# Kernel optimization log

Hardware: AMD Instinct MI355X
Metric: run time of the kernel (lower is better)

## Reference

```python
import jax, jax.numpy as jnp
import numpy as np
import math

N_NODES = 100000
N_EDGES = 1600000
IN_DIM = 32
OUT_DIM = 32

def setup_inputs() -> dict:
    key = jax.random.key(0)
    k1, k2, k3, k4 = jax.random.split(key, 4)
    X = jax.random.normal(k1, (N_NODES, IN_DIM), dtype=jnp.float32)
    src_idx = jax.random.randint(k2, (N_EDGES,), 0, N_NODES, dtype=jnp.int64)
    dst_idx = jax.random.randint(k3, (N_EDGES,), 0, N_NODES, dtype=jnp.int64)
    # weights init: uniform(-stdv, stdv), stdv = 1/sqrt(output_dim)
    stdv = 1.0 / math.sqrt(OUT_DIM)
    W = jax.random.uniform(k4, (IN_DIM, OUT_DIM), dtype=jnp.float32,
                           minval=-stdv, maxval=stdv)
    return {"X": X, "W": W, "src_idx": src_idx, "dst_idx": dst_idx}

def reference(X, W, src_idx, dst_idx):
    # GIN sum-aggregation SpMM: agg[i] = sum_{j in N(i)} X[j]
    agg = jax.ops.segment_sum(X[src_idx], dst_idx, num_segments=N_NODES)
    # dense GEMM: X_prime = agg @ W
    return agg @ W
```

## Files before the change

### kernel.cpp

```cpp
#include <hip/hip_runtime.h>

#define N_DIM 32
#define NPB 64
#define NB_FINE_MAX 2048
#define NC_MAX 128
#define CSH 10
#define CAPC 18432
#define CAPFINE 1280
#define CEPB 4096
#define FT 512
#define GROWS 512
#define CAPF 2048
#define MAXCH 10

__device__ __forceinline__ unsigned f2bf_rne(float f) {
    unsigned u = __float_as_uint(f);
    return (u + 0x7FFFu + ((u >> 16) & 1u)) >> 16;
}
__device__ __forceinline__ float bf2f(unsigned h) {
    return __uint_as_float(h << 16);
}

__global__ __launch_bounds__(FT) void k_fused(const float* __restrict__ X,
                                              const float* __restrict__ W,
                                              unsigned* __restrict__ Y,
                                              const int* __restrict__ src,
                                              const int* __restrict__ dst,
                                              int* __restrict__ cursorC0,
                                              int* __restrict__ tmp,
                                              int n_nodes, int n_edges,
                                              int ncoarse, int nblk_g) {
    __shared__ float Wlds[N_DIM * N_DIM];
    __shared__ int h[NC_MAX];
    __shared__ int gb[NC_MAX];
    const int t = threadIdx.x;

    if (blockIdx.x < nblk_g) {
        for (int i = t; i < N_DIM * N_DIM; i += FT) Wlds[i] = W[i];
        __syncthreads();
        const int r = blockIdx.x * GROWS + t;
        if (r >= n_nodes) return;

        float x[N_DIM];
        const float4* xr = (const float4*)(X + (size_t)r * N_DIM);
#pragma unroll
        for (int i = 0; i < N_DIM / 4; ++i) {
            float4 v = xr[i];
            x[4 * i + 0] = v.x; x[4 * i + 1] = v.y;
            x[4 * i + 2] = v.z; x[4 * i + 3] = v.w;
        }
        float acc[N_DIM];
#pragma unroll
        for (int c = 0; c < N_DIM; ++c) acc[c] = 0.0f;
#pragma unroll
        for (int k = 0; k < N_DIM; ++k) {
            const float xk = x[k];
#pragma unroll
            for (int c = 0; c < N_DIM; ++c)
                acc[c] = fmaf(xk, Wlds[k * N_DIM + c], acc[c]);
        }
        unsigned yp[16];
#pragma unroll
        for (int q = 0; q < 16; ++q)
            yp[q] = f2bf_rne(acc[2 * q]) | (f2bf_rne(acc[2 * q + 1]) << 16);
        uint4* yr = (uint4*)(Y + (size_t)r * 16);
#pragma unroll
        for (int i = 0; i < 4; ++i)
            yr[i] = make_uint4(yp[4 * i], yp[4 * i + 1],
                               yp[4 * i + 2], yp[4 * i + 3]);
    } else {
        if (t < NC_MAX) h[t] = 0;
        __syncthreads();
        const int start = (blockIdx.x - nblk_g) * CEPB;

        int vw[CEPB / FT], cw[CEPB / FT], rw[CEPB / FT];
#pragma unroll
        for (int k = 0; k < CEPB / FT; ++k) {
            int e = start + t + k * FT;
            if (e < n_edges) {
                int d = dst[e];
                int c = d >> CSH;
                cw[k] = c;
                vw[k] = src[e] | ((d & 1023) << 17);
                rw[k] = atomicAdd(&h[c], 1);
            } else {
                cw[k] = -1;
            }
        }
        __syncthreads();
        if (t < ncoarse) {
            int c = h[t];
            gb[t] = c ? atomicAdd(&cursorC0[t], c) : 0;
        }
        __syncthreads();
#pragma unroll
        for (int k = 0; k < CEPB / FT; ++k)
            if (cw[k] >= 0) {
                int idx = gb[cw[k]] + rw[k];
                if (idx < CAPC) tmp[cw[k] * CAPC + idx] = vw[k];
            }
    }
}

__global__ __launch_bounds__(256) void k_fpart(const int* __restrict__ tmp,
                                               const int* __restrict__ cursorC0,
                                               int* __restrict__ cursorF0,
                                               int* __restrict__ pairs,
                                               int ncoarse) {
    __shared__ int cnt[16], gpos[16];
    const int t = threadIdx.x;
    const int c = blockIdx.x;
    const int lenC = min(cursorC0[c], CAPC);

    for (int chunk = blockIdx.y; chunk * CAPF < lenC; chunk += gridDim.y) {
        const int start = chunk * CAPF;
        const int n = min(CAPF, lenC - start);
        if (t < 16) cnt[t] = 0;
        __syncthreads();
        int pv[CAPF / 256], rv[CAPF / 256];
#pragma unroll
        for (int k = 0; k < CAPF / 256; ++k) {
            int i = t + k * 256;
            if (i < n) {
                int p = tmp[c * CAPC + start + i];
                pv[k] = p;
                rv[k] = atomicAdd(&cnt[(p >> 23) & 15], 1);
            } else {
                pv[k] = -1;
            }
        }
        __syncthreads();
        if (t < 16) gpos[t] = cnt[t] ? atomicAdd(&cursorF0[16 * c + t], cnt[t]) : 0;
        __syncthreads();
#pragma unroll
        for (int k = 0; k < CAPF / 256; ++k) {
            if (pv[k] >= 0) {
                int p = pv[k];
                int f = (p >> 23) & 15;
                int idx = gpos[f] + rv[k];
                if (idx < CAPFINE)
                    pairs[(size_t)(16 * c + f) * CAPFINE + idx] = p & 0x7FFFFF;
            }
        }
        __syncthreads();
    }
}

__device__ __forceinline__ void addv(float* acc, uint4 v) {
    acc[0] += bf2f(v.x & 0xFFFFu); acc[1] += bf2f(v.x >> 16);
    acc[2] += bf2f(v.y & 0xFFFFu); acc[3] += bf2f(v.y >> 16);
    acc[4] += bf2f(v.z & 0xFFFFu); acc[5] += bf2f(v.z >> 16);
    acc[6] += bf2f(v.w & 0xFFFFu); acc[7] += bf2f(v.w >> 16);
}

__global__ __launch_bounds__(256) void k_agg(const uint4* __restrict__ Y4,
                                             const int* __restrict__ cursorF0,
                                             const int* __restrict__ pairs,
                                             float* __restrict__ out,
                                             int n_nodes) {
    __shared__ int sbin[CAPFINE];
    __shared__ int cnt[NPB];
    __shared__ int cst[NPB];
    __shared__ int excl[NPB];

    const int t = threadIdx.x;
    const int b = blockIdx.x;
    const int len = min(cursorF0[b], CAPFINE);
    const size_t segbase = (size_t)b * CAPFINE;
    const int g = t >> 2;
    const int l = t & 3;

    if (t < NPB) cnt[t] = 0;
    __syncthreads();

    int pv[CAPFINE / 256], rv[CAPFINE / 256];
#pragma unroll
    for (int k = 0; k < CAPFINE / 256; ++k) {
        int i = t + k * 256;
        if (i < len) {
            int p = pairs[segbase + i];
            pv[k] = p;
            rv[k] = atomicAdd(&cnt[p >> 17], 1);
        } else {
            pv[k] = -1;
        }
    }
    __syncthreads();
    if (t < 64) {
        int c0 = cnt[t];
        int c = c0;
#pragma unroll
        for (int off = 1; off < 64; off <<= 1) {
            int u = __shfl_up(c, off, 64);
            if (t >= off) c += u;
        }
        cst[t] = c;
        excl[t] = c - c0;
    }
    __syncthreads();
#pragma unroll
    for (int k = 0; k < CAPFINE / 256; ++k) {
        if (pv[k] >= 0) {
            int p = pv[k];
            sbin[excl[p >> 17] + rv[k]] = p & 0x1FFFF;
        }
    }
    __syncthreads();

    float acc[8];
#pragma unroll
    for (int i = 0; i < 8; ++i) acc[i] = 0.0f;

    const int s1 = cst[g];
    const int s0 = s1 - cnt[g];
    for (int e = s0; e < s1; e += 4) {
        const int m = s1 - e;
        int i0 = sbin[e];
        int i1 = sbin[e + ((m > 1) ? 1 : 0)];
        int i2 = sbin[e + ((m > 2) ? 2 : 0)];
        int i3 = sbin[e + ((m > 3) ? 3 : 0)];
        uint4 v0 = Y4[(size_t)i0 * 4 + l];
        uint4 v1 = Y4[(size_t)i1 * 4 + l];
        uint4 v2 = Y4[(size_t)i2 * 4 + l];
        uint4 v3 = Y4[(size_t)i3 * 4 + l];
        addv(acc, v0);
        if (m > 1) addv(acc, v1);
        if (m > 2) addv(acc, v2);
        if (m > 3) addv(acc, v3);
    }

    const int node = b * NPB + g;
    if (node < n_nodes) {
        ((float4*)out)[(size_t)node * 8 + 2 * l] =
            make_float4(acc[0], acc[1], acc[2], acc[3]);
        ((float4*)out)[(size_t)node * 8 + 2 * l + 1] =
            make_float4(acc[4], acc[5], acc[6], acc[7]);
    }
}

extern "C" void kernel_launch(void* const* d_in, const int* in_sizes, int n_in,
                              void* d_out, int out_size, void* d_ws, size_t ws_size,
                              hipStream_t stream) {
    const float* X   = (const float*)d_in[0];
    const float* W   = (const float*)d_in[1];
    const int*   src = (const int*)d_in[2];
    const int*   dst = (const int*)d_in[3];
    float* out = (float*)d_out;

    const int n_nodes = in_sizes[0] / N_DIM;
    const int n_edges = in_sizes[2];
    const int nb = (n_nodes + NPB - 1) / NPB;
    const int ncoarse = (n_nodes + 1023) / 1024;

    unsigned* Y   = (unsigned*)d_ws;
    int* cursorC0 = (int*)(Y + (size_t)n_nodes * 16);
    int* cursorF0 = cursorC0 + NC_MAX;
    int* tmp      = cursorF0 + NB_FINE_MAX;
    int* pairs    = tmp + (size_t)ncoarse * CAPC;

    const int nblk_g = (n_nodes + GROWS - 1) / GROWS;
    const int nblk_c = (n_edges + CEPB - 1) / CEPB;

    hipMemsetAsync(cursorC0, 0, (size_t)(NC_MAX + NB_FINE_MAX) * sizeof(int), stream);

    k_fused<<<nblk_g + nblk_c, FT, 0, stream>>>(X, W, Y, src, dst, cursorC0, tmp,
                                                n_nodes, n_edges, ncoarse, nblk_g);
    k_fpart<<<dim3(ncoarse, MAXCH), 256, 0, stream>>>(tmp, cursorC0, cursorF0,
                                                      pairs, ncoarse);
    k_agg<<<nb, 256, 0, stream>>>((const uint4*)Y, cursorF0, pairs, out, n_nodes);
}
```

Measured before the change: 126.3 us.

## Fuse fine partition into aggregation by filtering coarse buckets per block

Removes the separate fine-partition kernel and its pairs buffer and cursor array. Each aggregation block now scans its whole coarse bucket with vectorized loads and keeps only the entries whose fine bin matches, compacting them into shared memory via a shared atomic counter before the existing local bin sort and gather. This removes a launch, the global atomics and the intermediate global write/read. In exchange, each coarse bucket is read 16 times redundantly, which relies on cache hits.

After: 128.7 us. Within noise of the previous version (+1.8%).

```diff
diff --git a/kernel.cpp b/kernel.cpp
--- a/kernel.cpp
+++ b/kernel.cpp
@@ -2,7 +2,6 @@
 
 #define N_DIM 32
 #define NPB 64
-#define NB_FINE_MAX 2048
 #define NC_MAX 128
 #define CSH 10
 #define CAPC 18432
@@ -10,8 +9,7 @@
 #define CEPB 4096
 #define FT 512
 #define GROWS 512
-#define CAPF 2048
-#define MAXCH 10
+#define BT 256
 
 __device__ __forceinline__ unsigned f2bf_rne(float f) {
     unsigned u = __float_as_uint(f);
@@ -19,6 +17,12 @@
 }
 __device__ __forceinline__ float bf2f(unsigned h) {
     return __uint_as_float(h << 16);
+}
+__device__ __forceinline__ void addv(float* acc, uint4 v) {
+    acc[0] += bf2f(v.x & 0xFFFFu); acc[1] += bf2f(v.x >> 16);
+    acc[2] += bf2f(v.y & 0xFFFFu); acc[3] += bf2f(v.y >> 16);
+    acc[4] += bf2f(v.z & 0xFFFFu); acc[5] += bf2f(v.z >> 16);
+    acc[6] += bf2f(v.w & 0xFFFFu); acc[7] += bf2f(v.w >> 16);
 }
 
 __global__ __launch_bounds__(FT) void k_fused(const float* __restrict__ X,
@@ -102,117 +106,93 @@
     }
 }
 
-__global__ __launch_bounds__(256) void k_fpart(const int* __restrict__ tmp,
-                                               const int* __restrict__ cursorC0,
-                                               int* __restrict__ cursorF0,
-                                               int* __restrict__ pairs,
-                                               int ncoarse) {
-    __shared__ int cnt[16], gpos[16];
-    const int t = threadIdx.x;
-    const int c = blockIdx.x;
-    const int lenC = min(cursorC0[c], CAPC);
-
-    for (int chunk = blockIdx.y; chunk * CAPF < lenC; chunk += gridDim.y) {
-        const int start = chunk * CAPF;
-        const int n = min(CAPF, lenC - start);
-        if (t < 16) cnt[t] = 0;
-        __syncthreads();
-        int pv[CAPF / 256], rv[CAPF / 256];
-#pragma unroll
-        for (int k = 0; k < CAPF / 256; ++k) {
-            int i = t + k * 256;
-            if (i < n) {
-                int p = tmp[c * CAPC + start + i];
-                pv[k] = p;
-                rv[k] = atomicAdd(&cnt[(p >> 23) & 15], 1);
-            } else {
-                pv[k] = -1;
-            }
-        }
-        __syncthreads();
-        if (t < 16) gpos[t] = cnt[t] ? atomicAdd(&cursorF0[16 * c + t], cnt[t]) : 0;
-        __syncthreads();
-#pragma unroll
-        for (int k = 0; k < CAPF / 256; ++k) {
-            if (pv[k] >= 0) {
-                int p = pv[k];
-                int f = (p >> 23) & 15;
-                int idx = gpos[f] + rv[k];
-                if (idx < CAPFINE)
-                    pairs[(size_t)(16 * c + f) * CAPFINE + idx] = p & 0x7FFFFF;
-            }
-        }
-        __syncthreads();
-    }
-}
-
-__device__ __forceinline__ void addv(float* acc, uint4 v) {
-    acc[0] += bf2f(v.x & 0xFFFFu); acc[1] += bf2f(v.x >> 16);
-    acc[2] += bf2f(v.y & 0xFFFFu); acc[3] += bf2f(v.y >> 16);
-    acc[4] += bf2f(v.z & 0xFFFFu); acc[5] += bf2f(v.z >> 16);
-    acc[6] += bf2f(v.w & 0xFFFFu); acc[7] += bf2f(v.w >> 16);
-}
-
-__global__ __launch_bounds__(256) void k_agg(const uint4* __restrict__ Y4,
-                                             const int* __restrict__ cursorF0,
-                                             const int* __restrict__ pairs,
+__global__ __launch_bounds__(BT) void k_agg2(const uint4* __restrict__ Y4,
+                                             const int* __restrict__ cursorC0,
+                                             const int* __restrict__ tmp,
                                              float* __restrict__ out,
                                              int n_nodes) {
+    __shared__ int raw[CAPFINE];
     __shared__ int sbin[CAPFINE];
-    __shared__ int cnt[NPB];
-    __shared__ int cst[NPB];
-    __shared__ int excl[NPB];
+    __shared__ int cnt64[NPB], cst64[NPB], excl64[NPB];
+    __shared__ int ucnt;
 
     const int t = threadIdx.x;
     const int b = blockIdx.x;
-    const int len = min(cursorF0[b], CAPFINE);
-    const size_t segbase = (size_t)b * CAPFINE;
+    const int c = b >> 4;
+    const int f = b & 15;
+    const int lenC = min(cursorC0[c], CAPC);
+
+    if (t == 0) ucnt = 0;
+    __syncthreads();
+
+    const int* seg = tmp + c * CAPC;
+    const int nv4 = lenC >> 2;
+    const int4* seg4 = (const int4*)seg;
+    for (int i = t; i < nv4; i += BT) {
+        int4 q = seg4[i];
+#pragma unroll
+        for (int j = 0; j < 4; ++j) {
+            int p = (j == 0) ? q.x : (j == 1) ? q.y : (j == 2) ? q.z : q.w;
+            if (((p >> 23) & 15) == f) {
+                int r = atomicAdd(&ucnt, 1);
+                if (r < CAPFINE) raw[r] = p & 0x7FFFFF;
+            }
+        }
+    }
+    for (int i = 4 * nv4 + t; i < lenC; i += BT) {
+        int p = seg[i];
+        if (((p >> 23) & 15) == f) {
+            int r = atomicAdd(&ucnt, 1);
+            if (r < CAPFINE) raw[r] = p & 0x7FFFFF;
+        }
+    }
+    __syncthreads();
+    const int len = min(ucnt, CAPFINE);
+
+    if (t < NPB) cnt64[t] = 0;
+    __syncthreads();
+    int pv[CAPFINE / BT], rv[CAPFINE / BT];
+#pragma unroll
+    for (int k = 0; k < CAPFINE / BT; ++k) {
+        int i = t + k * BT;
+        if (i < len) {
+            int p = raw[i];
+            pv[k] = p;
+            rv[k] = atomicAdd(&cnt64[p >> 17], 1);
+        } else {
+            pv[k] = -1;
+        }
+    }
+    __syncthreads();
+    if (t < 64) {
+        int c0 = cnt64[t];
+        int cc = c0;
+#pragma unroll
+        for (int off = 1; off < 64; off <<= 1) {
+            int u = __shfl_up(cc, off, 64);
+            if (t >= off) cc += u;
+        }
+        cst64[t] = cc;
+        excl64[t] = cc - c0;
+    }
+    __syncthreads();
+#pragma unroll
+    for (int k = 0; k < CAPFINE / BT; ++k) {
+        if (pv[k] >= 0) {
+            int p = pv[k];
+            sbin[excl64[p >> 17] + rv[k]] = p & 0x1FFFF;
+        }
+    }
+    __syncthreads();
+
     const int g = t >> 2;
     const int l = t & 3;
-
-    if (t < NPB) cnt[t] = 0;
-    __syncthreads();
-
-    int pv[CAPFINE / 256], rv[CAPFINE / 256];
-#pragma unroll
-    for (int k = 0; k < CAPFINE / 256; ++k) {
-        int i = t + k * 256;
-        if (i < len) {
-            int p = pairs[segbase + i];
-            pv[k] = p;
-            rv[k] = atomicAdd(&cnt[p >> 17], 1);
-        } else {
-            pv[k] = -1;
-        }
-    }
-    __syncthreads();
-    if (t < 64) {
-        int c0 = cnt[t];
-        int c = c0;
-#pragma unroll
-        for (int off = 1; off < 64; off <<= 1) {
-            int u = __shfl_up(c, off, 64);
-            if (t >= off) c += u;
-        }
-        cst[t] = c;
-        excl[t] = c - c0;
-    }
-    __syncthreads();
-#pragma unroll
-    for (int k = 0; k < CAPFINE / 256; ++k) {
-        if (pv[k] >= 0) {
-            int p = pv[k];
-            sbin[excl[p >> 17] + rv[k]] = p & 0x1FFFF;
-        }
-    }
-    __syncthreads();
-
     float acc[8];
 #pragma unroll
     for (int i = 0; i < 8; ++i) acc[i] = 0.0f;
 
-    const int s1 = cst[g];
-    const int s0 = s1 - cnt[g];
+    const int s1 = cst64[g];
+    const int s0 = s1 - cnt64[g];
     for (int e = s0; e < s1; e += 4) {
         const int m = s1 - e;
         int i0 = sbin[e];
@@ -229,7 +209,7 @@
         if (m > 3) addv(acc, v3);
     }
 
-    const int node = b * NPB + g;
+    const int node = c * 1024 + f * 64 + g;
     if (node < n_nodes) {
         ((float4*)out)[(size_t)node * 8 + 2 * l] =
             make_float4(acc[0], acc[1], acc[2], acc[3]);
@@ -249,23 +229,19 @@
 
     const int n_nodes = in_sizes[0] / N_DIM;
     const int n_edges = in_sizes[2];
-    const int nb = (n_nodes + NPB - 1) / NPB;
     const int ncoarse = (n_nodes + 1023) / 1024;
 
     unsigned* Y   = (unsigned*)d_ws;
     int* cursorC0 = (int*)(Y + (size_t)n_nodes * 16);
-    int* cursorF0 = cursorC0 + NC_MAX;
-    int* tmp      = cursorF0 + NB_FINE_MAX;
-    int* pairs    = tmp + (size_t)ncoarse * CAPC;
+    int* tmp      = cursorC0 + NC_MAX;
 
     const int nblk_g = (n_nodes + GROWS - 1) / GROWS;
     const int nblk_c = (n_edges + CEPB - 1) / CEPB;
 
-    hipMemsetAsync(cursorC0, 0, (size_t)(NC_MAX + NB_FINE_MAX) * sizeof(int), stream);
+    hipMemsetAsync(cursorC0, 0, (size_t)NC_MAX * sizeof(int), stream);
 
     k_fused<<<nblk_g + nblk_c, FT, 0, stream>>>(X, W, Y, src, dst, cursorC0, tmp,
                                                 n_nodes, n_edges, ncoarse, nblk_g);
-    k_fpart<<<dim3(ncoarse, MAXCH), 256, 0, stream>>>(tmp, cursorC0, cursorF0,
-                                                      pairs, ncoarse);
-    k_agg<<<nb, 256, 0, stream>>>((const uint4*)Y, cursorF0, pairs, out, n_nodes);
-}
+    k_agg2<<<ncoarse * 16, BT, 0, stream>>>((const uint4*)Y, cursorC0, tmp,
+                                            out, n_nodes);
+}
```
